# Kernel optimization log

Measured on AMD Instinct MI355X. Metric: run time of the kernel, lower is better.

The kernel has to match this reference:

```python
import jax, jax.numpy as jnp
import numpy as np
import math

DIM = 2048
N_HEADS = 16
N_KV_HEADS = 8
HEAD_DIM = DIM // N_HEADS  # 128
N_REP = N_HEADS // N_KV_HEADS  # 2
SEQ = 2048
BATCH = 1
HIDDEN = 5632  # round_up(int(2*(4*2048)/3), 256)
NORM_EPS = 1e-5
LN_EPS = 1e-5  # torch.nn.LayerNorm default
ROPE_THETA = 10000.0


def rmsnorm(x, w, eps=NORM_EPS):
    x32 = x.astype(jnp.float32)
    n = x32 * jax.lax.rsqrt(jnp.mean(x32 * x32, axis=-1, keepdims=True) + eps)
    return n.astype(x.dtype) * w


def layernorm(x, w, b, eps=LN_EPS):
    mu = jnp.mean(x, axis=-1, keepdims=True)
    var = jnp.mean((x - mu) ** 2, axis=-1, keepdims=True)
    return (x - mu) * jax.lax.rsqrt(var + eps) * w + b


def apply_rope(x, cos, sin):
    # x: [B,S,H,hd]; cos/sin: [S, hd//2] -> complex multiply on (even, odd) pairs
    xr = x.reshape(*x.shape[:-1], HEAD_DIM // 2, 2)
    x0, x1 = xr[..., 0], xr[..., 1]
    c = cos[None, :, None, :]
    s = sin[None, :, None, :]
    o0 = x0 * c - x1 * s
    o1 = x0 * s + x1 * c
    return jnp.stack([o0, o1], axis=-1).reshape(x.shape)


def setup_inputs() -> dict:
    key = jax.random.key(0)
    ks = jax.random.split(key, 10)
    scale = 0.02
    x = jax.random.normal(ks[0], (BATCH, SEQ, DIM), jnp.float32)
    # RoPE tables
    inv_freq = 1.0 / (ROPE_THETA ** (jnp.arange(0, HEAD_DIM, 2, dtype=jnp.float32) / HEAD_DIM))
    ang = jnp.arange(SEQ, dtype=jnp.float32)[:, None] * inv_freq[None, :]  # [S, hd//2]
    freqs_cos = jnp.cos(ang)
    freqs_sin = jnp.sin(ang)
    # causal additive mask
    mask = jnp.where(jnp.tril(jnp.ones((SEQ, SEQ), bool)), 0.0, -1e9).astype(jnp.float32)
    wqkv = jax.random.normal(ks[1], ((N_HEADS + 2 * N_KV_HEADS) * HEAD_DIM, DIM), jnp.float32) * scale
    wo = jax.random.normal(ks[2], (DIM, N_HEADS * HEAD_DIM), jnp.float32) * scale
    qn_w = jnp.ones((HEAD_DIM,), jnp.float32)
    qn_b = jnp.zeros((HEAD_DIM,), jnp.float32)
    kn_w = jnp.ones((HEAD_DIM,), jnp.float32)
    kn_b = jnp.zeros((HEAD_DIM,), jnp.float32)
    attn_norm_w = jnp.ones((DIM,), jnp.float32)
    ffn_norm_w = jnp.ones((DIM,), jnp.float32)
    w13 = jax.random.normal(ks[3], (2 * HIDDEN, DIM), jnp.float32) * scale
    w2 = jax.random.normal(ks[4], (DIM, HIDDEN), jnp.float32) * scale
    return dict(x=x, freqs_cos=freqs_cos, freqs_sin=freqs_sin, mask=mask,
                wqkv=wqkv, wo=wo, qn_w=qn_w, qn_b=qn_b, kn_w=kn_w, kn_b=kn_b,
                attn_norm_w=attn_norm_w, ffn_norm_w=ffn_norm_w, w13=w13, w2=w2)


def reference(x, freqs_cos, freqs_sin, mask, wqkv, wo, qn_w, qn_b, kn_w, kn_b,
              attn_norm_w, ffn_norm_w, w13, w2):
    B, S, _ = x.shape
    # ---- attention sublayer (pre-norm) ----
    h = rmsnorm(x, attn_norm_w)
    qkv = h @ wqkv.T  # [B,S,(H+2KV)*hd]
    q_sz = N_HEADS * HEAD_DIM
    kv_sz = N_KV_HEADS * HEAD_DIM
    q = qkv[..., :q_sz].reshape(B, S, N_HEADS, HEAD_DIM)
    k = qkv[..., q_sz:q_sz + kv_sz].reshape(B, S, N_KV_HEADS, HEAD_DIM)
    v = qkv[..., q_sz + kv_sz:].reshape(B, S, N_KV_HEADS, HEAD_DIM)
    # QK-LayerNorm (per head_dim)
    q = layernorm(q, qn_w, qn_b)
    k = layernorm(k, kn_w, kn_b)
    # RoPE
    q = apply_rope(q, freqs_cos, freqs_sin)
    k = apply_rope(k, freqs_cos, freqs_sin)
    # GQA: repeat kv heads (interleaved like torch repeat_interleave on head dim)
    k = jnp.repeat(k, N_REP, axis=2)
    v = jnp.repeat(v, N_REP, axis=2)
    # scores with fp32 softmax
    scores = jnp.einsum('bqhd,bkhd->bhqk', q, k) / math.sqrt(HEAD_DIM)
    scores = scores + mask[None, None, :, :]
    p = jax.nn.softmax(scores.astype(jnp.float32), axis=-1).astype(q.dtype)
    o = jnp.einsum('bhqk,bkhd->bqhd', p, v).reshape(B, S, N_HEADS * HEAD_DIM)
    attn_out = o @ wo.T
    h = x + attn_out
    # ---- SwiGLU FFN sublayer ----
    g = rmsnorm(h, ffn_norm_w)
    x13 = g @ w13.T
    x1, x3 = x13[..., :HIDDEN], x13[..., HIDDEN:]
    out = h + (jax.nn.silu(x1) * x3) @ w2.T
    return out
```

## Files before the change

kernel.cpp:

```cpp
#include <hip/hip_runtime.h>
#include <math.h>

#define DIM 2048
#define SEQ 2048
#define NH 16
#define NKV 8
#define HD 128
#define HIDDEN 5632
#define QKV_N 4096
#define FF_N 11264

typedef __attribute__((ext_vector_type(8))) short s16x8;
typedef __attribute__((ext_vector_type(4))) float f32x4;

#define GPTR(p) ((const __attribute__((address_space(1))) void*)(p))
#define LPTR(p) ((__attribute__((address_space(3))) void*)(p))

#define CFENCE() __asm__ __volatile__("" ::: "memory")
#define BAR() do { CFENCE(); __builtin_amdgcn_s_barrier(); CFENCE(); } while (0)

__device__ __forceinline__ unsigned short f2bf(float f) {
    union { float f; unsigned u; } v; v.f = f;
    unsigned r = v.u + 0x7fff + ((v.u >> 16) & 1);
    return (unsigned short)(r >> 16);
}
__device__ __forceinline__ float bf2f(unsigned short s) {
    union { unsigned u; float f; } v; v.u = ((unsigned)s) << 16;
    return v.f;
}

__global__ __launch_bounds__(256) void k_cvt(const float* __restrict__ src,
                                             unsigned short* __restrict__ dst, int n4) {
    int i = blockIdx.x * 256 + threadIdx.x;
    if (i < n4) {
        float4 v = ((const float4*)src)[i];
        ushort4 o;
        o.x = f2bf(v.x); o.y = f2bf(v.y); o.z = f2bf(v.z); o.w = f2bf(v.w);
        ((ushort4*)dst)[i] = o;
    }
}

__global__ __launch_bounds__(256) void k_rmsnorm(const float* __restrict__ x,
                                                 const float* __restrict__ w,
                                                 unsigned short* __restrict__ out) {
    int row = blockIdx.x;
    int tid = threadIdx.x, wv = tid >> 6, lane = tid & 63;
    const float* xr = x + (size_t)row * DIM;
    float4 a = ((const float4*)xr)[tid * 2];
    float4 b = ((const float4*)xr)[tid * 2 + 1];
    float ss = a.x*a.x + a.y*a.y + a.z*a.z + a.w*a.w
             + b.x*b.x + b.y*b.y + b.z*b.z + b.w*b.w;
    for (int off = 32; off >= 1; off >>= 1) ss += __shfl_xor(ss, off);
    __shared__ float red[4];
    if (lane == 0) red[wv] = ss;
    __syncthreads();
    float tot = red[0] + red[1] + red[2] + red[3];
    float rs = rsqrtf(tot * (1.0f / DIM) + 1e-5f);
    float4 wa = ((const float4*)w)[tid * 2];
    float4 wb = ((const float4*)w)[tid * 2 + 1];
    ushort4 o0, o1;
    o0.x = f2bf(a.x * rs * wa.x); o0.y = f2bf(a.y * rs * wa.y);
    o0.z = f2bf(a.z * rs * wa.z); o0.w = f2bf(a.w * rs * wa.w);
    o1.x = f2bf(b.x * rs * wb.x); o1.y = f2bf(b.y * rs * wb.y);
    o1.z = f2bf(b.z * rs * wb.z); o1.w = f2bf(b.w * rs * wb.w);
    ushort4* orow = (ushort4*)(out + (size_t)row * DIM);
    orow[tid * 2] = o0; orow[tid * 2 + 1] = o1;
}

template<int ID>
__global__ __launch_bounds__(512, 2) void k_gemm256(
    const unsigned short* __restrict__ A, const unsigned short* __restrict__ B,
    int M, int N, int K, int Kslice,
    float* __restrict__ Cf, unsigned short* __restrict__ Cb,
    const float* __restrict__ add, int flags) {
    __shared__ __align__(16) unsigned short As[2][16384];
    __shared__ __align__(16) unsigned short Bs[2][16384];
    int tid = threadIdx.x;
    int wv = tid >> 6, lane = tid & 63, quad = lane >> 4, l15 = lane & 15;
    int wr = wv >> 2, wc = wv & 3;

    int gx = gridDim.x, gy = gridDim.y;
    int n_wg = gx * gy * gridDim.z;
    int lin = (blockIdx.z * gy + blockIdx.y) * gx + blockIdx.x;
    int q8 = n_wg >> 3, r8 = n_wg & 7;
    int xcd = lin & 7, idx8 = lin >> 3;
    int nl = (xcd < r8 ? xcd * (q8 + 1) : r8 * (q8 + 1) + (xcd - r8) * q8) + idx8;
    int bx = nl % gx; int rest = nl / gx;
    int by = rest % gy; int bz = rest / gy;

    int rowBase = by * 256;
    int colBase = bx * 256;
    int kb = bz * Kslice;
    int NT = Kslice >> 6;

    f32x4 acc[8][4] = {};

    int srow = lane >> 3;
    int schunk = lane & 7;

    auto stage = [&](const unsigned short* Mat, int matBase,
                     unsigned short (*Ls)[16384], int t, int h, int b) {
#pragma unroll
        for (int j = 0; j < 2; j++) {
            int r0 = h * 128 + (j * 8 + wv) * 8;
            int row = r0 + srow;
            int kchunk = schunk ^ (row & 7);
            const unsigned short* g = Mat + (size_t)(matBase + row) * K
                                      + (kb + t * 64 + kchunk * 8);
            __builtin_amdgcn_global_load_lds(GPTR(g), LPTR(&Ls[b][r0 * 64]), 16, 0, 0);
        }
    };
    auto LDA = [&](int b_, int mt, int ks) -> s16x8 {
        int row = wr * 128 + mt * 16 + l15;
        return *(const s16x8*)&As[b_][row * 64 + ((((ks * 4 + quad)) ^ (row & 7)) << 3)];
    };
    auto LDB = [&](int b_, int nt, int ks) -> s16x8 {
        int row = wc * 64 + nt * 16 + l15;
        return *(const s16x8*)&Bs[b_][row * 64 + ((((ks * 4 + quad)) ^ (row & 7)) << 3)];
    };

    stage(B, colBase, Bs, 0, 0, 0); stage(B, colBase, Bs, 0, 1, 0);
    stage(A, rowBase, As, 0, 0, 0); stage(A, rowBase, As, 0, 1, 0);
    if (NT > 1) {
        stage(B, colBase, Bs, 1, 0, 1); stage(B, colBase, Bs, 1, 1, 1);
        stage(A, rowBase, As, 1, 0, 1); stage(A, rowBase, As, 1, 1, 1);
        asm volatile("s_waitcnt vmcnt(8)" ::: "memory");
    } else {
        asm volatile("s_waitcnt vmcnt(0)" ::: "memory");
    }
    BAR();

    for (int T = 0; T < NT; T++) {
        const int b = T & 1;
        s16x8 a0[8], b0[4], b1[4];
#pragma unroll
        for (int nt = 0; nt < 4; nt++) b0[nt] = LDB(b, nt, 0);
#pragma unroll
        for (int mt = 0; mt < 8; mt++) a0[mt] = LDA(b, mt, 0);
#pragma unroll
        for (int nt = 0; nt < 4; nt++) b1[nt] = LDB(b, nt, 1);
        __builtin_amdgcn_s_setprio(1);
#pragma unroll
        for (int mt = 0; mt < 8; mt++) {
            acc[mt][0] = __builtin_amdgcn_mfma_f32_16x16x32_bf16(a0[mt], b0[0], acc[mt][0], 0, 0, 0);
            acc[mt][1] = __builtin_amdgcn_mfma_f32_16x16x32_bf16(a0[mt], b0[1], acc[mt][1], 0, 0, 0);
            acc[mt][2] = __builtin_amdgcn_mfma_f32_16x16x32_bf16(a0[mt], b0[2], acc[mt][2], 0, 0, 0);
            acc[mt][3] = __builtin_amdgcn_mfma_f32_16x16x32_bf16(a0[mt], b0[3], acc[mt][3], 0, 0, 0);
        }
        __builtin_amdgcn_s_setprio(0);
        s16x8 a1[8];
#pragma unroll
        for (int mt = 0; mt < 8; mt++) a1[mt] = LDA(b, mt, 1);
        asm volatile("s_waitcnt lgkmcnt(0)" ::: "memory");
        BAR();
        if (T + 2 < NT) {
            stage(B, colBase, Bs, T + 2, 0, b); stage(B, colBase, Bs, T + 2, 1, b);
            stage(A, rowBase, As, T + 2, 0, b); stage(A, rowBase, As, T + 2, 1, b);
        }
        __builtin_amdgcn_s_setprio(1);
#pragma unroll
        for (int mt = 0; mt < 8; mt++) {
            acc[mt][0] = __builtin_amdgcn_mfma_f32_16x16x32_bf16(a1[mt], b1[0], acc[mt][0], 0, 0, 0);
            acc[mt][1] = __builtin_amdgcn_mfma_f32_16x16x32_bf16(a1[mt], b1[1], acc[mt][1], 0, 0, 0);
            acc[mt][2] = __builtin_amdgcn_mfma_f32_16x16x32_bf16(a1[mt], b1[2], acc[mt][2], 0, 0, 0);
            acc[mt][3] = __builtin_amdgcn_mfma_f32_16x16x32_bf16(a1[mt], b1[3], acc[mt][3], 0, 0, 0);
        }
        __builtin_amdgcn_s_setprio(0);
        if (T + 2 < NT) asm volatile("s_waitcnt vmcnt(8)" ::: "memory");
        else            asm volatile("s_waitcnt vmcnt(0)" ::: "memory");
        BAR();
    }

    float* Cfz = Cf ? Cf + (size_t)bz * M * N : nullptr;
#pragma unroll
    for (int mt = 0; mt < 8; mt++)
#pragma unroll
        for (int nt = 0; nt < 4; nt++)
#pragma unroll
            for (int r = 0; r < 4; r++) {
                int row = rowBase + wr * 128 + mt * 16 + quad * 4 + r;
                int col = colBase + wc * 64 + nt * 16 + l15;
                size_t idx = (size_t)row * N + col;
                float v = acc[mt][nt][r];
                if (flags == 1) v += add[idx];
                if (flags == 2) Cb[idx] = f2bf(v);
                else            Cfz[idx] = v;
            }
}

__global__ __launch_bounds__(256) void k_red5(const float* __restrict__ p,
                                              size_t pstride,
                                              const float* __restrict__ res,
                                              float* __restrict__ o, int n4) {
    int i = blockIdx.x * 256 + threadIdx.x;
    if (i < n4) {
        float4 r = ((const float4*)res)[i];
#pragma unroll
        for (int z = 0; z < 4; z++) {
            float4 v = ((const float4*)(p + z * pstride))[i];
            r.x += v.x; r.y += v.y; r.z += v.z; r.w += v.w;
        }
        ((float4*)o)[i] = r;
    }
}

__global__ __launch_bounds__(256) void k_qknorm_rope(
    const float* __restrict__ qkv0, const float* __restrict__ qkv1,
    const float* __restrict__ qw, const float* __restrict__ qb,
    const float* __restrict__ kw, const float* __restrict__ kb,
    const float* __restrict__ fcos, const float* __restrict__ fsin,
    unsigned short* __restrict__ qout, unsigned short* __restrict__ kfrag) {
    int wv = threadIdx.x >> 6, lane = threadIdx.x & 63;
    int hl = blockIdx.y;
    int s = blockIdx.x * 4 + wv;
    bool isq = hl < 16;
    size_t base = (size_t)s * QKV_N + hl * HD + 2 * lane;
    float2 u = *(const float2*)&qkv0[base];
    float2 w2v = *(const float2*)&qkv1[base];
    float2 xv; xv.x = u.x + w2v.x; xv.y = u.y + w2v.y;
    float sum = xv.x + xv.y, ssq = xv.x * xv.x + xv.y * xv.y;
    for (int off = 32; off >= 1; off >>= 1) {
        sum += __shfl_xor(sum, off);
        ssq += __shfl_xor(ssq, off);
    }
    float mu = sum * (1.0f / HD);
    float var = ssq * (1.0f / HD) - mu * mu;
    float rs = rsqrtf(var + 1e-5f);
    const float* w_ = isq ? qw : kw;
    const float* b_ = isq ? qb : kb;
    float n0 = (xv.x - mu) * rs * w_[2 * lane]     + b_[2 * lane];
    float n1 = (xv.y - mu) * rs * w_[2 * lane + 1] + b_[2 * lane + 1];
    float c = fcos[s * 64 + lane], sn = fsin[s * 64 + lane];
    float o0 = n0 * c - n1 * sn;
    float o1 = n0 * sn + n1 * c;
    if (isq) {
        const float sc = 0.12751744f;
        o0 *= sc; o1 *= sc;
        unsigned val = (unsigned)f2bf(o0) | ((unsigned)f2bf(o1) << 16);
        *(unsigned*)&qout[((size_t)hl * SEQ + s) * HD + 2 * lane] = val;
    } else {
        int kvh = hl - 16;
        int kt = s >> 6, key = s & 63;
        int dg = lane >> 2, j = (2 * lane) & 7;
        unsigned val = (unsigned)f2bf(o0) | ((unsigned)f2bf(o1) << 16);
        size_t idx = (((size_t)(kvh * 32 + kt) * 16 + dg) * 64 + key) * 8 + j;
        *(unsigned*)&kfrag[idx] = val;
    }
}

__global__ __launch_bounds__(256) void k_vprep(const float* __restrict__ qkv0,
                                               const float* __restrict__ qkv1,
                                               unsigned short* __restrict__ vfrag) {
    __shared__ unsigned short lv[64][132];
    int kvh = blockIdx.y, kt = blockIdx.x, tid = threadIdx.x;
#pragma unroll
    for (int it = 0; it < 8; it++) {
        int li = it * 256 + tid;
        int row = li >> 5;
        int c4 = (li & 31) * 4;
        size_t base = (size_t)(kt * 64 + row) * QKV_N + 3072 + kvh * HD + c4;
        float4 v = *(const float4*)&qkv0[base];
        float4 v1 = *(const float4*)&qkv1[base];
        v.x += v1.x; v.y += v1.y; v.z += v1.z; v.w += v1.w;
        lv[row][c4] = f2bf(v.x); lv[row][c4 + 1] = f2bf(v.y);
        lv[row][c4 + 2] = f2bf(v.z); lv[row][c4 + 3] = f2bf(v.w);
    }
    __syncthreads();
    size_t base = (size_t)(kvh * 32 + kt) * 8192;
#pragma unroll
    for (int it = 0; it < 16; it++) {
        int o2 = it * 256 + tid;
        int e = o2 * 2;
        int r = e & 7, d = (e >> 3) & 127, kg = e >> 10;
        unsigned val = (unsigned)lv[kg * 8 + r][d] | ((unsigned)lv[kg * 8 + r + 1][d] << 16);
        *(unsigned*)&vfrag[base + e] = val;
    }
}

__global__ __launch_bounds__(256) void k_flash(
    const unsigned short* __restrict__ q,
    const unsigned short* __restrict__ kfrag,
    const unsigned short* __restrict__ vfrag,
    unsigned short* __restrict__ o) {
    __shared__ __align__(16) unsigned short Ks[2][8192];
    __shared__ __align__(16) unsigned short Vs[2][8192];
    __shared__ __align__(16) unsigned short Ps[4][16 * 72];
    int h = blockIdx.x & 15;
    int qt = 31 - (blockIdx.x >> 4);
    int kvh = h >> 1;
    int tid = threadIdx.x, wv = tid >> 6, lane = tid & 63, quad = lane >> 4, l15 = lane & 15;
    int qbase = qt * 64;

    s16x8 qf[4];
    {
        const unsigned short* qp = q + ((size_t)h * SEQ + qbase + wv * 16 + l15) * HD + quad * 8;
#pragma unroll
        for (int ks = 0; ks < 4; ks++) qf[ks] = *(const s16x8*)(qp + ks * 32);
    }
    f32x4 oacc[8] = {};
    float mst[4], lst[4];
#pragma unroll
    for (int r = 0; r < 4; r++) { mst[r] = -3e38f; lst[r] = 0.f; }

    auto issueKV = [&](int kt, int b) {
        size_t kb = (size_t)(kvh * 32 + kt) * 8192;
#pragma unroll
        for (int i = 0; i < 4; i++) {
            int s0 = i * 256 + wv * 64;
            __builtin_amdgcn_global_load_lds(GPTR(kfrag + kb + (size_t)(s0 + lane) * 8), LPTR(&Ks[b][s0 * 8]), 16, 0, 0);
            __builtin_amdgcn_global_load_lds(GPTR(vfrag + kb + (size_t)(s0 + lane) * 8), LPTR(&Vs[b][s0 * 8]), 16, 0, 0);
        }
    };

    issueKV(0, 0);
    for (int kt = 0; kt <= qt; kt++) {
        int b = kt & 1;
        __syncthreads();
        if (kt < qt) issueKV(kt + 1, b ^ 1);

        f32x4 sacc[4];
#pragma unroll
        for (int nt = 0; nt < 4; nt++) {
            f32x4 a = {};
#pragma unroll
            for (int ks = 0; ks < 4; ks++) {
                s16x8 kf = *(const s16x8*)&Ks[b][((ks * 4 + quad) * 64 + nt * 16 + l15) * 8];
                a = __builtin_amdgcn_mfma_f32_16x16x32_bf16(qf[ks], kf, a, 0, 0, 0);
            }
            sacc[nt] = a;
        }
        if (kt == qt) {
#pragma unroll
            for (int nt = 0; nt < 4; nt++) {
                int colg = kt * 64 + nt * 16 + l15;
#pragma unroll
                for (int r = 0; r < 4; r++) {
                    int rowg = qbase + wv * 16 + quad * 4 + r;
                    if (colg > rowg) sacc[nt][r] = -3e38f;
                }
            }
        }
        unsigned short* Pw = Ps[wv];
#pragma unroll
        for (int r = 0; r < 4; r++) {
            float mx = fmaxf(fmaxf(sacc[0][r], sacc[1][r]), fmaxf(sacc[2][r], sacc[3][r]));
#pragma unroll
            for (int off = 1; off < 16; off <<= 1) mx = fmaxf(mx, __shfl_xor(mx, off));
            float mnew = fmaxf(mst[r], mx);
            float alpha = exp2f(mst[r] - mnew);
            float psum = 0.f;
#pragma unroll
            for (int nt = 0; nt < 4; nt++) {
                float p = exp2f(sacc[nt][r] - mnew);
                psum += p;
                Pw[(quad * 4 + r) * 72 + nt * 16 + l15] = f2bf(p);
            }
#pragma unroll
            for (int off = 1; off < 16; off <<= 1) psum += __shfl_xor(psum, off);
            lst[r] = lst[r] * alpha + psum;
            mst[r] = mnew;
#pragma unroll
            for (int vt = 0; vt < 8; vt++) oacc[vt][r] *= alpha;
        }
#pragma unroll
        for (int ks = 0; ks < 2; ks++) {
            s16x8 pf = *(const s16x8*)&Pw[l15 * 72 + ks * 32 + quad * 8];
#pragma unroll
            for (int vt = 0; vt < 8; vt++) {
                s16x8 vf = *(const s16x8*)&Vs[b][((ks * 4 + quad) * 128 + vt * 16 + l15) * 8];
                oacc[vt] = __builtin_amdgcn_mfma_f32_16x16x32_bf16(pf, vf, oacc[vt], 0, 0, 0);
            }
        }
    }
#pragma unroll
    for (int r = 0; r < 4; r++) {
        float inv = 1.0f / lst[r];
        int row = qbase + wv * 16 + quad * 4 + r;
#pragma unroll
        for (int vt = 0; vt < 8; vt++)
            o[(size_t)row * DIM + h * HD + vt * 16 + l15] = f2bf(oacc[vt][r] * inv);
    }
}

__global__ __launch_bounds__(256) void k_silu(const unsigned short* __restrict__ x13,
                                              unsigned short* __restrict__ y) {
    int gid = blockIdx.x * 256 + threadIdx.x;
    int s = gid / 1408;
    int j4 = (gid - s * 1408) * 4;
    const unsigned short* p1 = x13 + (size_t)s * FF_N + j4;
    const unsigned short* p3 = p1 + HIDDEN;
    ushort4 a = *(const ushort4*)p1;
    ushort4 b = *(const ushort4*)p3;
    ushort4 o;
    {
        float x1 = bf2f(a.x), x3 = bf2f(b.x);
        o.x = f2bf(x1 / (1.f + __expf(-x1)) * x3);
    }
    {
        float x1 = bf2f(a.y), x3 = bf2f(b.y);
        o.y = f2bf(x1 / (1.f + __expf(-x1)) * x3);
    }
    {
        float x1 = bf2f(a.z), x3 = bf2f(b.z);
        o.z = f2bf(x1 / (1.f + __expf(-x1)) * x3);
    }
    {
        float x1 = bf2f(a.w), x3 = bf2f(b.w);
        o.w = f2bf(x1 / (1.f + __expf(-x1)) * x3);
    }
    *(ushort4*)&y[(size_t)s * HIDDEN + j4] = o;
}

extern "C" void kernel_launch(void* const* d_in, const int* in_sizes, int n_in,
                              void* d_out, int out_size, void* d_ws, size_t ws_size,
                              hipStream_t stream) {
    const float* x    = (const float*)d_in[0];
    const float* fcos = (const float*)d_in[1];
    const float* fsin = (const float*)d_in[2];
    const float* wqkv = (const float*)d_in[4];
    const float* wo   = (const float*)d_in[5];
    const float* qn_w = (const float*)d_in[6];
    const float* qn_b = (const float*)d_in[7];
    const float* kn_w = (const float*)d_in[8];
    const float* kn_b = (const float*)d_in[9];
    const float* anw  = (const float*)d_in[10];
    const float* fnw  = (const float*)d_in[11];
    const float* w13  = (const float*)d_in[12];
    const float* w2   = (const float*)d_in[13];
    float* out = (float*)d_out;
    char* ws = (char*)d_ws;

    size_t off = 0;
    auto alloc = [&](size_t bytes) { size_t o = off; off += (bytes + 255) & ~(size_t)255; return o; };
    unsigned short* wqkv_b = (unsigned short*)(ws + alloc((size_t)QKV_N * DIM * 2));
    unsigned short* wo_b   = (unsigned short*)(ws + alloc((size_t)DIM * DIM * 2));
    unsigned short* w13_b  = (unsigned short*)(ws + alloc((size_t)FF_N * DIM * 2));
    unsigned short* w2_b   = (unsigned short*)(ws + alloc((size_t)DIM * HIDDEN * 2));
    unsigned short* xn     = (unsigned short*)(ws + alloc((size_t)SEQ * DIM * 2));
    unsigned short* qb_    = (unsigned short*)(ws + alloc((size_t)NH * SEQ * HD * 2));
    unsigned short* kfr    = (unsigned short*)(ws + alloc((size_t)NKV * SEQ * HD * 2));
    unsigned short* vfr    = (unsigned short*)(ws + alloc((size_t)NKV * SEQ * HD * 2));
    unsigned short* ob     = (unsigned short*)(ws + alloc((size_t)SEQ * DIM * 2));
    float*          hbuf   = (float*)         (ws + alloc((size_t)SEQ * DIM * 4));
    unsigned short* gb     = (unsigned short*)(ws + alloc((size_t)SEQ * DIM * 2));
    unsigned short* x13b   = (unsigned short*)(ws + alloc((size_t)SEQ * FF_N * 2));
    unsigned short* yb     = (unsigned short*)(ws + alloc((size_t)SEQ * HIDDEN * 2));
    float*          pp     = (float*)         (ws + alloc((size_t)4 * SEQ * DIM * 4));
    const size_t pstride = (size_t)SEQ * DIM;
    float* qkvp  = pp;
    const float* qkvp1 = qkvp + (size_t)SEQ * QKV_N;

    k_cvt<<<8192, 256, 0, stream>>>(wqkv, wqkv_b, QKV_N * DIM / 4);
    k_cvt<<<4096, 256, 0, stream>>>(wo, wo_b, DIM * DIM / 4);
    k_cvt<<<22528, 256, 0, stream>>>(w13, w13_b, FF_N * DIM / 4);
    k_cvt<<<11264, 256, 0, stream>>>(w2, w2_b, DIM * HIDDEN / 4);

    k_rmsnorm<<<SEQ, 256, 0, stream>>>(x, anw, xn);
    k_gemm256<0><<<dim3(QKV_N / 256, SEQ / 256, 2), 512, 0, stream>>>(
        xn, wqkv_b, SEQ, QKV_N, DIM, DIM / 2, qkvp, nullptr, nullptr, 0);
    k_qknorm_rope<<<dim3(SEQ / 4, NH + NKV), 256, 0, stream>>>(
        qkvp, qkvp1, qn_w, qn_b, kn_w, kn_b, fcos, fsin, qb_, kfr);
    k_vprep<<<dim3(SEQ / 64, NKV), 256, 0, stream>>>(qkvp, qkvp1, vfr);
    k_flash<<<NH * (SEQ / 64), 256, 0, stream>>>(qb_, kfr, vfr, ob);
    k_gemm256<1><<<dim3(DIM / 256, SEQ / 256, 4), 512, 0, stream>>>(
        ob, wo_b, SEQ, DIM, DIM, DIM / 4, pp, nullptr, nullptr, 0);
    k_red5<<<SEQ * DIM / 1024, 256, 0, stream>>>(pp, pstride, x, hbuf, SEQ * DIM / 4);
    k_rmsnorm<<<SEQ, 256, 0, stream>>>(hbuf, fnw, gb);
    k_gemm256<2><<<dim3(FF_N / 256, SEQ / 256), 512, 0, stream>>>(
        gb, w13_b, SEQ, FF_N, DIM, DIM, nullptr, x13b, nullptr, 2);
    k_silu<<<SEQ * (HIDDEN / 4) / 256, 256, 0, stream>>>(x13b, yb);
    k_gemm256<3><<<dim3(DIM / 256, SEQ / 256, 4), 512, 0, stream>>>(
        yb, w2_b, SEQ, DIM, HIDDEN, HIDDEN / 4, pp, nullptr, nullptr, 0);
    k_red5<<<SEQ * DIM / 1024, 256, 0, stream>>>(pp, pstride, hbuf, out, SEQ * DIM / 4);
}
```

Measured before the change: 677.8 us.

## Fuse SiLU-gate into W13 GEMM epilogue, fuse residual reduce with RMSNorm, drop XCD remap

```diff
diff --git a/kernel.cpp b/kernel.cpp
--- a/kernel.cpp
+++ b/kernel.cpp
@@ -38,6 +38,18 @@
         o.x = f2bf(v.x); o.y = f2bf(v.y); o.z = f2bf(v.z); o.w = f2bf(v.w);
         ((ushort4*)dst)[i] = o;
     }
+}
+
+__global__ __launch_bounds__(256) void k_cvt13(const float* __restrict__ src,
+                                               unsigned short* __restrict__ dst) {
+    int i = blockIdx.x * 256 + threadIdx.x;
+    int r = i >> 9, c4 = i & 511;
+    int j = (r < HIDDEN) ? r : r - HIDDEN;
+    int np = ((j >> 3) << 4) + (j & 7) + ((r < HIDDEN) ? 0 : 8);
+    float4 v = ((const float4*)src)[i];
+    ushort4 o;
+    o.x = f2bf(v.x); o.y = f2bf(v.y); o.z = f2bf(v.z); o.w = f2bf(v.w);
+    ((ushort4*)dst)[np * 512 + c4] = o;
 }
 
 __global__ __launch_bounds__(256) void k_rmsnorm(const float* __restrict__ x,
@@ -67,6 +79,45 @@
     orow[tid * 2] = o0; orow[tid * 2 + 1] = o1;
 }
 
+__global__ __launch_bounds__(256) void k_rednorm(const float* __restrict__ p,
+                                                 size_t pstride,
+                                                 const float* __restrict__ res,
+                                                 const float* __restrict__ w,
+                                                 float* __restrict__ hout,
+                                                 unsigned short* __restrict__ nout) {
+    int row = blockIdx.x;
+    int tid = threadIdx.x, wv = tid >> 6, lane = tid & 63;
+    size_t base = (size_t)row * DIM;
+    float4 a = ((const float4*)(res + base))[tid * 2];
+    float4 b = ((const float4*)(res + base))[tid * 2 + 1];
+#pragma unroll
+    for (int z = 0; z < 4; z++) {
+        float4 u = ((const float4*)(p + z * pstride + base))[tid * 2];
+        float4 v = ((const float4*)(p + z * pstride + base))[tid * 2 + 1];
+        a.x += u.x; a.y += u.y; a.z += u.z; a.w += u.w;
+        b.x += v.x; b.y += v.y; b.z += v.z; b.w += v.w;
+    }
+    ((float4*)(hout + base))[tid * 2] = a;
+    ((float4*)(hout + base))[tid * 2 + 1] = b;
+    float ss = a.x*a.x + a.y*a.y + a.z*a.z + a.w*a.w
+             + b.x*b.x + b.y*b.y + b.z*b.z + b.w*b.w;
+    for (int off = 32; off >= 1; off >>= 1) ss += __shfl_xor(ss, off);
+    __shared__ float red[4];
+    if (lane == 0) red[wv] = ss;
+    __syncthreads();
+    float tot = red[0] + red[1] + red[2] + red[3];
+    float rs = rsqrtf(tot * (1.0f / DIM) + 1e-5f);
+    float4 wa = ((const float4*)w)[tid * 2];
+    float4 wb = ((const float4*)w)[tid * 2 + 1];
+    ushort4 o0, o1;
+    o0.x = f2bf(a.x * rs * wa.x); o0.y = f2bf(a.y * rs * wa.y);
+    o0.z = f2bf(a.z * rs * wa.z); o0.w = f2bf(a.w * rs * wa.w);
+    o1.x = f2bf(b.x * rs * wb.x); o1.y = f2bf(b.y * rs * wb.y);
+    o1.z = f2bf(b.z * rs * wb.z); o1.w = f2bf(b.w * rs * wb.w);
+    ushort4* orow = (ushort4*)(nout + base);
+    orow[tid * 2] = o0; orow[tid * 2 + 1] = o1;
+}
+
 template<int ID>
 __global__ __launch_bounds__(512, 2) void k_gemm256(
     const unsigned short* __restrict__ A, const unsigned short* __restrict__ B,
@@ -79,18 +130,9 @@
     int wv = tid >> 6, lane = tid & 63, quad = lane >> 4, l15 = lane & 15;
     int wr = wv >> 2, wc = wv & 3;
 
-    int gx = gridDim.x, gy = gridDim.y;
-    int n_wg = gx * gy * gridDim.z;
-    int lin = (blockIdx.z * gy + blockIdx.y) * gx + blockIdx.x;
-    int q8 = n_wg >> 3, r8 = n_wg & 7;
-    int xcd = lin & 7, idx8 = lin >> 3;
-    int nl = (xcd < r8 ? xcd * (q8 + 1) : r8 * (q8 + 1) + (xcd - r8) * q8) + idx8;
-    int bx = nl % gx; int rest = nl / gx;
-    int by = rest % gy; int bz = rest / gy;
-
-    int rowBase = by * 256;
-    int colBase = bx * 256;
-    int kb = bz * Kslice;
+    int rowBase = blockIdx.y * 256;
+    int colBase = blockIdx.x * 256;
+    int kb = blockIdx.z * Kslice;
     int NT = Kslice >> 6;
 
     f32x4 acc[8][4] = {};
@@ -171,21 +213,40 @@
         BAR();
     }
 
-    float* Cfz = Cf ? Cf + (size_t)bz * M * N : nullptr;
-#pragma unroll
-    for (int mt = 0; mt < 8; mt++)
-#pragma unroll
-        for (int nt = 0; nt < 4; nt++)
-#pragma unroll
-            for (int r = 0; r < 4; r++) {
-                int row = rowBase + wr * 128 + mt * 16 + quad * 4 + r;
-                int col = colBase + wc * 64 + nt * 16 + l15;
-                size_t idx = (size_t)row * N + col;
-                float v = acc[mt][nt][r];
-                if (flags == 1) v += add[idx];
-                if (flags == 2) Cb[idx] = f2bf(v);
-                else            Cfz[idx] = v;
+    if (flags == 3) {
+#pragma unroll
+        for (int mt = 0; mt < 8; mt++)
+#pragma unroll
+            for (int nt = 0; nt < 4; nt++) {
+                int g = (colBase + wc * 64 + nt * 16) >> 4;
+#pragma unroll
+                for (int r = 0; r < 4; r++) {
+                    int row = rowBase + wr * 128 + mt * 16 + quad * 4 + r;
+                    float v = acc[mt][nt][r];
+                    float prt = __shfl_xor(v, 8);
+                    if (l15 < 8) {
+                        float y = v / (1.f + __expf(-v)) * prt;
+                        Cb[(size_t)row * HIDDEN + g * 8 + l15] = f2bf(y);
+                    }
+                }
             }
+    } else {
+        float* Cfz = Cf ? Cf + (size_t)blockIdx.z * M * N : nullptr;
+#pragma unroll
+        for (int mt = 0; mt < 8; mt++)
+#pragma unroll
+            for (int nt = 0; nt < 4; nt++)
+#pragma unroll
+                for (int r = 0; r < 4; r++) {
+                    int row = rowBase + wr * 128 + mt * 16 + quad * 4 + r;
+                    int col = colBase + wc * 64 + nt * 16 + l15;
+                    size_t idx = (size_t)row * N + col;
+                    float v = acc[mt][nt][r];
+                    if (flags == 1) v += add[idx];
+                    if (flags == 2) Cb[idx] = f2bf(v);
+                    else            Cfz[idx] = v;
+                }
+    }
 }
 
 __global__ __launch_bounds__(256) void k_red5(const float* __restrict__ p,
@@ -382,35 +443,6 @@
     }
 }
 
-__global__ __launch_bounds__(256) void k_silu(const unsigned short* __restrict__ x13,
-                                              unsigned short* __restrict__ y) {
-    int gid = blockIdx.x * 256 + threadIdx.x;
-    int s = gid / 1408;
-    int j4 = (gid - s * 1408) * 4;
-    const unsigned short* p1 = x13 + (size_t)s * FF_N + j4;
-    const unsigned short* p3 = p1 + HIDDEN;
-    ushort4 a = *(const ushort4*)p1;
-    ushort4 b = *(const ushort4*)p3;
-    ushort4 o;
-    {
-        float x1 = bf2f(a.x), x3 = bf2f(b.x);
-        o.x = f2bf(x1 / (1.f + __expf(-x1)) * x3);
-    }
-    {
-        float x1 = bf2f(a.y), x3 = bf2f(b.y);
-        o.y = f2bf(x1 / (1.f + __expf(-x1)) * x3);
-    }
-    {
-        float x1 = bf2f(a.z), x3 = bf2f(b.z);
-        o.z = f2bf(x1 / (1.f + __expf(-x1)) * x3);
-    }
-    {
-        float x1 = bf2f(a.w), x3 = bf2f(b.w);
-        o.w = f2bf(x1 / (1.f + __expf(-x1)) * x3);
-    }
-    *(ushort4*)&y[(size_t)s * HIDDEN + j4] = o;
-}
-
 extern "C" void kernel_launch(void* const* d_in, const int* in_sizes, int n_in,
                               void* d_out, int out_size, void* d_ws, size_t ws_size,
                               hipStream_t stream) {
@@ -443,7 +475,6 @@
     unsigned short* ob     = (unsigned short*)(ws + alloc((size_t)SEQ * DIM * 2));
     float*          hbuf   = (float*)         (ws + alloc((size_t)SEQ * DIM * 4));
     unsigned short* gb     = (unsigned short*)(ws + alloc((size_t)SEQ * DIM * 2));
-    unsigned short* x13b   = (unsigned short*)(ws + alloc((size_t)SEQ * FF_N * 2));
     unsigned short* yb     = (unsigned short*)(ws + alloc((size_t)SEQ * HIDDEN * 2));
     float*          pp     = (float*)         (ws + alloc((size_t)4 * SEQ * DIM * 4));
     const size_t pstride = (size_t)SEQ * DIM;
@@ -452,7 +483,7 @@
 
     k_cvt<<<8192, 256, 0, stream>>>(wqkv, wqkv_b, QKV_N * DIM / 4);
     k_cvt<<<4096, 256, 0, stream>>>(wo, wo_b, DIM * DIM / 4);
-    k_cvt<<<22528, 256, 0, stream>>>(w13, w13_b, FF_N * DIM / 4);
+    k_cvt13<<<22528, 256, 0, stream>>>(w13, w13_b);
     k_cvt<<<11264, 256, 0, stream>>>(w2, w2_b, DIM * HIDDEN / 4);
 
     k_rmsnorm<<<SEQ, 256, 0, stream>>>(x, anw, xn);
@@ -464,11 +495,9 @@
     k_flash<<<NH * (SEQ / 64), 256, 0, stream>>>(qb_, kfr, vfr, ob);
     k_gemm256<1><<<dim3(DIM / 256, SEQ / 256, 4), 512, 0, stream>>>(
         ob, wo_b, SEQ, DIM, DIM, DIM / 4, pp, nullptr, nullptr, 0);
-    k_red5<<<SEQ * DIM / 1024, 256, 0, stream>>>(pp, pstride, x, hbuf, SEQ * DIM / 4);
-    k_rmsnorm<<<SEQ, 256, 0, stream>>>(hbuf, fnw, gb);
+    k_rednorm<<<SEQ, 256, 0, stream>>>(pp, pstride, x, fnw, hbuf, gb);
     k_gemm256<2><<<dim3(FF_N / 256, SEQ / 256), 512, 0, stream>>>(
-        gb, w13_b, SEQ, FF_N, DIM, DIM, nullptr, x13b, nullptr, 2);
-    k_silu<<<SEQ * (HIDDEN / 4) / 256, 256, 0, stream>>>(x13b, yb);
+        gb, w13_b, SEQ, FF_N, DIM, DIM, nullptr, yb, nullptr, 3);
     k_gemm256<3><<<dim3(DIM / 256, SEQ / 256, 4), 512, 0, stream>>>(
         yb, w2_b, SEQ, DIM, HIDDEN, HIDDEN / 4, pp, nullptr, nullptr, 0);
     k_red5<<<SEQ * DIM / 1024, 256, 0, stream>>>(pp, pstride, hbuf, out, SEQ * DIM / 4);
```

Result: faster. 657.9 us (-2.9%).
